# Kernel tuning notes

Hardware: AMD Instinct MI355X
Metric: run time of the kernel (lower is better)

The kernel has to match this reference:

```python
import jax, jax.numpy as jnp
import numpy as np


def setup_inputs() -> dict:
    key = jax.random.key(0)
    k1, k2, k3 = jax.random.split(key, 3)
    Lq, Lkv, H, D = 2048, 2048, 16, 128
    return {
        "query": jax.random.normal(k1, (Lq, H, D), dtype=jnp.float32),
        "key": jax.random.normal(k2, (Lkv, H, D), dtype=jnp.float32),
        "value": jax.random.normal(k3, (Lkv, H, D), dtype=jnp.float32),
    }


def reference(query, key, value):
    # query: [Lq, H, D], key: [Lkv, H, D], value: [Lkv, H, Dv]
    # Original module performs chunked online-softmax attention; the math is
    # exactly scaled-dot-product softmax attention with scale 1/sqrt(k_features).
    d = query.shape[-1]
    q = query * (1.0 / jnp.sqrt(jnp.asarray(d, dtype=query.dtype)))
    scores = jnp.einsum('qhd,khd->qhk', q, key)          # [Lq, H, Lkv]
    weights = jax.nn.softmax(scores, axis=-1)            # numerically stable online softmax equivalent
    out = jnp.einsum('qhk,khf->qhf', weights, value)     # [Lq, H, Dv]
    return out
```

## Files before the change

kernel.cpp:

```cpp
#include <hip/hip_runtime.h>
#include <hip/hip_bf16.h>

typedef __bf16 bf16x8 __attribute__((ext_vector_type(8)));
typedef __bf16 bf16x4 __attribute__((ext_vector_type(4)));
typedef float  f32x16 __attribute__((ext_vector_type(16)));
typedef float  f32x4  __attribute__((ext_vector_type(4)));

#define HD      2048
#define DH      128
#define KVT     64
#define NCH     16
#define NSPLIT  2
#define NROWS   32768
#define KTILE_E 8192
#define VTILE_E 8704

__device__ __forceinline__ void glds16(const void* g, void* l) {
    typedef const __attribute__((address_space(1))) void g_as_t;
    typedef __attribute__((address_space(3))) void l_as_t;
    __builtin_amdgcn_global_load_lds((g_as_t*)g, (l_as_t*)l, 16, 0, 0);
}

__device__ __forceinline__ int kkey_of(int r) {
    return (r & 7) ^ (((r >> 3) & 3) << 1);
}

__global__ __launch_bounds__(256, 4)
void prep_kv(const float* __restrict__ Kg, const float* __restrict__ Vg,
             __bf16* __restrict__ wsK, __bf16* __restrict__ wsV)
{
    __shared__ float tile[32][33];
    const int bid = blockIdx.x;
    if (bid < 2048) {
        const int kv = bid;
        const int t  = threadIdx.x;
        const int h  = t >> 4, c8 = t & 15;
        const float* src = Kg + (size_t)kv * HD + h * DH + c8 * 8;
        f32x4 a = *(const f32x4*)(src);
        f32x4 b = *(const f32x4*)(src + 4);
        bf16x8 o;
        o[0]=(__bf16)a[0]; o[1]=(__bf16)a[1]; o[2]=(__bf16)a[2]; o[3]=(__bf16)a[3];
        o[4]=(__bf16)b[0]; o[5]=(__bf16)b[1]; o[6]=(__bf16)b[2]; o[7]=(__bf16)b[3];
        const int r = kv & 63;
        __bf16* dst = wsK + ((size_t)(h * 32 + (kv >> 6)) * KTILE_E)
                          + r * 128 + ((c8 ^ kkey_of(r)) << 3);
        *(bf16x8*)dst = o;
    } else {
        const int b = bid - 2048;
        const int dvb = b & 3, kvb = (b >> 2) & 63, h = b >> 8;
        const int t = threadIdx.x;
        {
            const int kvl = t >> 3, dv4 = (t & 7) * 4;
            f32x4 v = *(const f32x4*)(Vg + (size_t)(kvb * 32 + kvl) * HD + h * DH + dvb * 32 + dv4);
            tile[kvl][dv4 + 0] = v[0]; tile[kvl][dv4 + 1] = v[1];
            tile[kvl][dv4 + 2] = v[2]; tile[kvl][dv4 + 3] = v[3];
        }
        __syncthreads();
        {
            const int dvl = t >> 3, kv4 = (t & 7) * 4;
            const int dv   = dvb * 32 + dvl;
            const int T    = kvb >> 1;
            const int kloc = (kvb & 1) * 32 + kv4;
            bf16x4 o;
            o[0] = (__bf16)tile[kv4 + 0][dvl]; o[1] = (__bf16)tile[kv4 + 1][dvl];
            o[2] = (__bf16)tile[kv4 + 2][dvl]; o[3] = (__bf16)tile[kv4 + 3][dvl];
            __bf16* dst = wsV + ((size_t)(h * 32 + T) * VTILE_E) + dv * 68 + kloc;
            *(bf16x4*)dst = o;
        }
    }
}

__global__ __launch_bounds__(256, 2)
void fmha_main(const float* __restrict__ Qg,
               const __bf16* __restrict__ wsK, const __bf16* __restrict__ wsV,
               float* __restrict__ wsO, float* __restrict__ wsML)
{
    __shared__ __align__(16) __bf16 klds[2][KTILE_E];
    __shared__ __align__(16) __bf16 vlds[2][VTILE_E];

    const int tid  = threadIdx.x;
    const int lane = tid & 63;
    const int wrp  = tid >> 6;
    const int g    = lane >> 5;
    const int l31  = lane & 31;

    const int b    = blockIdx.x;
    const int grp  = b & 31;
    const int qblk = b >> 5;
    const int h    = grp >> 1;
    const int sp   = grp & 1;
    const int T0   = sp * NCH;

    const float qscale = 1.4426950408889634f * 0.08838834764831845f;
    const int q = qblk * 128 + wrp * 32 + l31;

    bf16x8 qf[8];
    {
        const float* qrow = Qg + (size_t)q * HD + h * DH;
        #pragma unroll
        for (int j = 0; j < 8; ++j) {
            f32x4 a = *(const f32x4*)(qrow + j * 16 + 8 * g);
            f32x4 c = *(const f32x4*)(qrow + j * 16 + 8 * g + 4);
            bf16x8 f;
            f[0] = (__bf16)(a[0] * qscale); f[1] = (__bf16)(a[1] * qscale);
            f[2] = (__bf16)(a[2] * qscale); f[3] = (__bf16)(a[3] * qscale);
            f[4] = (__bf16)(c[0] * qscale); f[5] = (__bf16)(c[1] * qscale);
            f[6] = (__bf16)(c[2] * qscale); f[7] = (__bf16)(c[3] * qscale);
            qf[j] = f;
        }
    }

    auto stage = [&](int T, int buf) {
        const char* kt = (const char*)(wsK + (size_t)(h * 32 + T) * KTILE_E) + wrp * 1024 + lane * 16;
        char* kl = (char*)&klds[buf][0] + wrp * 1024;
        #pragma unroll
        for (int i = 0; i < 4; ++i) glds16(kt + i * 4096, kl + i * 4096);
        const char* vt = (const char*)(wsV + (size_t)(h * 32 + T) * VTILE_E) + wrp * 1024 + lane * 16;
        char* vl = (char*)&vlds[buf][0] + wrp * 1024;
        #pragma unroll
        for (int i = 0; i < 4; ++i) glds16(vt + i * 4096, vl + i * 4096);
        if (wrp == 0) glds16(vt + 16384, vl + 16384);
    };

    auto sync_all = []() {
        asm volatile("s_waitcnt vmcnt(0) lgkmcnt(0)" ::: "memory");
        __builtin_amdgcn_s_barrier();
    };

    float mrun = -1e30f, lrun = 0.0f;
    f32x16 o0, o1, o2, o3;
    #pragma unroll
    for (int r = 0; r < 16; ++r) { o0[r] = 0.f; o1[r] = 0.f; o2[r] = 0.f; o3[r] = 0.f; }

    stage(T0, 0);
    sync_all();

    const int kkey = kkey_of(l31);

    #pragma unroll 2
    for (int tt = 0; tt < NCH; ++tt) {
        const int cur = tt & 1;
        if (tt + 1 < NCH) stage(T0 + tt + 1, cur ^ 1);

        f32x16 s0, s1;
        #pragma unroll
        for (int r = 0; r < 16; ++r) { s0[r] = 0.f; s1[r] = 0.f; }
        __builtin_amdgcn_s_setprio(1);
        #pragma unroll
        for (int j = 0; j < 8; ++j) {
            const int gcol = ((2 * j + g) ^ kkey) << 3;
            bf16x8 k0 = *(const bf16x8*)&klds[cur][l31 * 128 + gcol];
            s0 = __builtin_amdgcn_mfma_f32_32x32x16_bf16(k0, qf[j], s0, 0, 0, 0);
            bf16x8 k1 = *(const bf16x8*)&klds[cur][(32 + l31) * 128 + gcol];
            s1 = __builtin_amdgcn_mfma_f32_32x32x16_bf16(k1, qf[j], s1, 0, 0, 0);
        }
        __builtin_amdgcn_s_setprio(0);

        float m16[8];
        #pragma unroll
        for (int r = 0; r < 8; ++r)
            m16[r] = fmaxf(fmaxf(s0[r], s0[r + 8]), fmaxf(s1[r], s1[r + 8]));
        float tmax = fmaxf(fmaxf(fmaxf(m16[0], m16[4]), fmaxf(m16[1], m16[5])),
                           fmaxf(fmaxf(m16[2], m16[6]), fmaxf(m16[3], m16[7])));
        tmax = fmaxf(tmax, __shfl_xor(tmax, 32, 64));

        if (__any(tmax > mrun + 8.0f)) {
            const float mnew  = fmaxf(mrun, tmax);
            const float alpha = __builtin_amdgcn_exp2f(mrun - mnew);
            lrun *= alpha;
            #pragma unroll
            for (int r = 0; r < 16; ++r) { o0[r]*=alpha; o1[r]*=alpha; o2[r]*=alpha; o3[r]*=alpha; }
            mrun = mnew;
        }

        #pragma unroll
        for (int r = 0; r < 16; ++r) {
            s0[r] = __builtin_amdgcn_exp2f(s0[r] - mrun);
            s1[r] = __builtin_amdgcn_exp2f(s1[r] - mrun);
        }
        float ps = 0.f;
        #pragma unroll
        for (int r = 0; r < 16; ++r) ps += s0[r] + s1[r];
        lrun += ps;

        bf16x8 pf0, pf1, pf2, pf3;
        #pragma unroll
        for (int e = 0; e < 8; ++e) {
            pf0[e] = (__bf16)s0[e]; pf1[e] = (__bf16)s0[8 + e];
            pf2[e] = (__bf16)s1[e]; pf3[e] = (__bf16)s1[8 + e];
        }

        __builtin_amdgcn_s_setprio(1);
        #pragma unroll
        for (int bb = 0; bb < 4; ++bb) {
            const __bf16* vb = &vlds[cur][(bb * 32 + l31) * 68];
            f32x16& oo = (bb == 0) ? o0 : (bb == 1) ? o1 : (bb == 2) ? o2 : o3;
            #define PVSTEP(base, pf)                                              \
            {                                                                     \
                bf16x4 a0 = *(const bf16x4*)(vb + (base) + 4 * g);                \
                bf16x4 a1 = *(const bf16x4*)(vb + (base) + 8 + 4 * g);            \
                bf16x8 va;                                                        \
                va[0]=a0[0]; va[1]=a0[1]; va[2]=a0[2]; va[3]=a0[3];               \
                va[4]=a1[0]; va[5]=a1[1]; va[6]=a1[2]; va[7]=a1[3];               \
                oo = __builtin_amdgcn_mfma_f32_32x32x16_bf16(va, pf, oo, 0, 0, 0);\
            }
            PVSTEP(0,  pf0) PVSTEP(16, pf1) PVSTEP(32, pf2) PVSTEP(48, pf3)
            #undef PVSTEP
        }
        __builtin_amdgcn_s_setprio(0);

        if (tt + 1 < NCH) sync_all();
    }

    const float ltot  = lrun + __shfl_xor(lrun, 32, 64);
    const int   rowid = q * 16 + h;

    float* orow = wsO + ((size_t)sp * NROWS + rowid) * 128;
    #pragma unroll
    for (int bb = 0; bb < 4; ++bb) {
        const f32x16& oo = (bb == 0) ? o0 : (bb == 1) ? o1 : (bb == 2) ? o2 : o3;
        #pragma unroll
        for (int jj = 0; jj < 4; ++jj) {
            f32x4 v;
            v[0] = oo[4*jj+0]; v[1] = oo[4*jj+1]; v[2] = oo[4*jj+2]; v[3] = oo[4*jj+3];
            *(f32x4*)(orow + bb * 32 + 8 * jj + 4 * g) = v;
        }
    }
    if (lane < 32) {
        float* ml = wsML + ((size_t)sp * NROWS + rowid) * 2;
        ml[0] = mrun;
        ml[1] = ltot;
    }
}

__global__ __launch_bounds__(256, 4)
void fmha_combine(const float* __restrict__ wsO, const float* __restrict__ wsML,
                  float* __restrict__ Og)
{
    const int tid   = threadIdx.x;
    const int rowid = blockIdx.x * 8 + (tid >> 5);
    const int c     = (tid & 31) * 4;

    float m[NSPLIT], l[NSPLIT];
    float M = -1e30f;
    #pragma unroll
    for (int s = 0; s < NSPLIT; ++s) {
        const float* ml = wsML + ((size_t)s * NROWS + rowid) * 2;
        m[s] = ml[0]; l[s] = ml[1];
        M = fmaxf(M, m[s]);
    }
    float L = 0.f, w[NSPLIT];
    #pragma unroll
    for (int s = 0; s < NSPLIT; ++s) {
        w[s] = __builtin_amdgcn_exp2f(m[s] - M);
        L += l[s] * w[s];
    }
    const float inv = 1.0f / L;

    f32x4 acc; acc[0]=0.f; acc[1]=0.f; acc[2]=0.f; acc[3]=0.f;
    #pragma unroll
    for (int s = 0; s < NSPLIT; ++s) {
        f32x4 v = *(const f32x4*)(wsO + ((size_t)s * NROWS + rowid) * 128 + c);
        acc[0] += v[0] * w[s]; acc[1] += v[1] * w[s];
        acc[2] += v[2] * w[s]; acc[3] += v[3] * w[s];
    }
    f32x4 r;
    r[0] = acc[0]*inv; r[1] = acc[1]*inv; r[2] = acc[2]*inv; r[3] = acc[3]*inv;
    *(f32x4*)(Og + (size_t)rowid * 128 + c) = r;
}

__global__ __launch_bounds__(256, 2)
void fmha_fb(const float* __restrict__ Qg, const float* __restrict__ Kg,
             const float* __restrict__ Vg, float* __restrict__ Og)
{
    __shared__ __align__(16) __bf16 klds[2][32 * 128];
    __shared__ __align__(16) __bf16 vtlds[2][DH * 36];

    const int tid  = threadIdx.x;
    const int lane = tid & 63;
    const int wrp  = tid >> 6;
    const int g    = lane >> 5;
    const int l31  = lane & 31;

    const int b    = blockIdx.x;
    const int h    = 2 * (b & 7) + ((b >> 3) >> 4);
    const int qblk = (b >> 3) & 15;

    const float qscale = 1.4426950408889634f * 0.08838834764831845f;
    const int q = qblk * 128 + wrp * 32 + l31;

    bf16x8 qf[8];
    {
        const float* qrow = Qg + (size_t)q * HD + h * DH;
        #pragma unroll
        for (int db = 0; db < 8; ++db) {
            f32x4 a = *(const f32x4*)(qrow + db * 16 + 8 * g);
            f32x4 c = *(const f32x4*)(qrow + db * 16 + 8 * g + 4);
            bf16x8 f;
            f[0] = (__bf16)(a[0] * qscale); f[1] = (__bf16)(a[1] * qscale);
            f[2] = (__bf16)(a[2] * qscale); f[3] = (__bf16)(a[3] * qscale);
            f[4] = (__bf16)(c[0] * qscale); f[5] = (__bf16)(c[1] * qscale);
            f[6] = (__bf16)(c[2] * qscale); f[7] = (__bf16)(c[3] * qscale);
            qf[db] = f;
        }
    }

    const int krow = tid >> 3, kc = tid & 7;
    const int vkv  = tid & 31, vdv0 = (tid >> 5) * 16;
    const float* kbase = Kg + (size_t)h * DH;
    const float* vbase = Vg + (size_t)h * DH;

    f32x4 kreg0, kreg1, kreg2, kreg3, vreg0, vreg1, vreg2, vreg3;

    auto stage_load = [&](int t) {
        const float* kp = kbase + (size_t)(t * 32 + krow) * HD + kc * 8;
        kreg0 = *(const f32x4*)(kp);
        kreg1 = *(const f32x4*)(kp + 4);
        kreg2 = *(const f32x4*)(kp + 64);
        kreg3 = *(const f32x4*)(kp + 68);
        const float* vp = vbase + (size_t)(t * 32 + vkv) * HD + vdv0;
        vreg0 = *(const f32x4*)(vp);
        vreg1 = *(const f32x4*)(vp + 4);
        vreg2 = *(const f32x4*)(vp + 8);
        vreg3 = *(const f32x4*)(vp + 12);
    };

    auto stage_write = [&](int buf) {
        bf16x8 k0, k1;
        k0[0]=(__bf16)kreg0[0]; k0[1]=(__bf16)kreg0[1]; k0[2]=(__bf16)kreg0[2]; k0[3]=(__bf16)kreg0[3];
        k0[4]=(__bf16)kreg1[0]; k0[5]=(__bf16)kreg1[1]; k0[6]=(__bf16)kreg1[2]; k0[7]=(__bf16)kreg1[3];
        k1[0]=(__bf16)kreg2[0]; k1[1]=(__bf16)kreg2[1]; k1[2]=(__bf16)kreg2[2]; k1[3]=(__bf16)kreg2[3];
        k1[4]=(__bf16)kreg3[0]; k1[5]=(__bf16)kreg3[1]; k1[6]=(__bf16)kreg3[2]; k1[7]=(__bf16)kreg3[3];
        const int swz = (krow & 7) << 3;
        *(bf16x8*)&klds[buf][krow * 128 + ((kc * 8) ^ swz)]      = k0;
        *(bf16x8*)&klds[buf][krow * 128 + ((kc * 8 + 64) ^ swz)] = k1;
        #pragma unroll
        for (int jj = 0; jj < 4; ++jj) {
            f32x4 vv = (jj == 0) ? vreg0 : (jj == 1) ? vreg1 : (jj == 2) ? vreg2 : vreg3;
            #pragma unroll
            for (int e = 0; e < 4; ++e)
                vtlds[buf][(vdv0 + jj * 4 + e) * 36 + vkv] = (__bf16)vv[e];
        }
    };

    float mrun = -1e30f, lrun = 0.0f;
    f32x16 o0, o1, o2, o3;
    #pragma unroll
    for (int r = 0; r < 16; ++r) { o0[r] = 0.f; o1[r] = 0.f; o2[r] = 0.f; o3[r] = 0.f; }

    stage_load(0);
    stage_write(0);

    for (int tt = 0; tt < 64; ++tt) {
        const int cur = tt & 1;
        if (tt + 1 < 64) stage_load(tt + 1);
        __syncthreads();

        f32x16 sa, sb;
        #pragma unroll
        for (int r = 0; r < 16; ++r) { sa[r] = 0.f; sb[r] = 0.f; }
        const int kswz = (l31 & 7) << 3;
        #pragma unroll
        for (int db = 0; db < 4; ++db) {
            bf16x8 kfa = *(const bf16x8*)&klds[cur][l31 * 128 + (((2*db)   * 16 + g * 8) ^ kswz)];
            sa = __builtin_amdgcn_mfma_f32_32x32x16_bf16(kfa, qf[2*db],   sa, 0, 0, 0);
            bf16x8 kfb = *(const bf16x8*)&klds[cur][l31 * 128 + (((2*db+1) * 16 + g * 8) ^ kswz)];
            sb = __builtin_amdgcn_mfma_f32_32x32x16_bf16(kfb, qf[2*db+1], sb, 0, 0, 0);
        }
        f32x16 s;
        #pragma unroll
        for (int r = 0; r < 16; ++r) s[r] = sa[r] + sb[r];

        float m8[8];
        #pragma unroll
        for (int r = 0; r < 8; ++r) m8[r] = fmaxf(s[r], s[r + 8]);
        float tmax = fmaxf(fmaxf(fmaxf(m8[0], m8[4]), fmaxf(m8[1], m8[5])),
                           fmaxf(fmaxf(m8[2], m8[6]), fmaxf(m8[3], m8[7])));
        tmax = fmaxf(tmax, __shfl_xor(tmax, 32, 64));

        if (__any(tmax > mrun + 8.0f)) {
            const float mnew  = fmaxf(mrun, tmax);
            const float alpha = __builtin_amdgcn_exp2f(mrun - mnew);
            lrun *= alpha;
            #pragma unroll
            for (int r = 0; r < 16; ++r) { o0[r] *= alpha; o1[r] *= alpha; o2[r] *= alpha; o3[r] *= alpha; }
            mrun = mnew;
        }

        float p[16];
        #pragma unroll
        for (int r = 0; r < 16; ++r) p[r] = __builtin_amdgcn_exp2f(s[r] - mrun);
        float ps0 = 0, ps1 = 0, ps2 = 0, ps3 = 0;
        #pragma unroll
        for (int r = 0; r < 4; ++r) { ps0 += p[r]; ps1 += p[r+4]; ps2 += p[r+8]; ps3 += p[r+12]; }
        lrun += ((ps0 + ps1) + (ps2 + ps3));

        bf16x8 pf0, pf1;
        #pragma unroll
        for (int e = 0; e < 8; ++e) { pf0[e] = (__bf16)p[e]; pf1[e] = (__bf16)p[8 + e]; }

        #pragma unroll
        for (int bb = 0; bb < 4; ++bb) {
            const __bf16* vb = &vtlds[cur][(bb * 32 + l31) * 36];
            bf16x4 a0 = *(const bf16x4*)(vb + 4 * g);
            bf16x4 a1 = *(const bf16x4*)(vb + 8 + 4 * g);
            bf16x8 va;
            va[0]=a0[0]; va[1]=a0[1]; va[2]=a0[2]; va[3]=a0[3];
            va[4]=a1[0]; va[5]=a1[1]; va[6]=a1[2]; va[7]=a1[3];
            f32x16& oo = (bb == 0) ? o0 : (bb == 1) ? o1 : (bb == 2) ? o2 : o3;
            oo = __builtin_amdgcn_mfma_f32_32x32x16_bf16(va, pf0, oo, 0, 0, 0);
            bf16x4 b0 = *(const bf16x4*)(vb + 16 + 4 * g);
            bf16x4 b1 = *(const bf16x4*)(vb + 24 + 4 * g);
            va[0]=b0[0]; va[1]=b0[1]; va[2]=b0[2]; va[3]=b0[3];
            va[4]=b1[0]; va[5]=b1[1]; va[6]=b1[2]; va[7]=b1[3];
            oo = __builtin_amdgcn_mfma_f32_32x32x16_bf16(va, pf1, oo, 0, 0, 0);
        }

        if (tt + 1 < 64) stage_write(cur ^ 1);
    }

    const float ltot = lrun + __shfl_xor(lrun, 32, 64);
    const float inv  = 1.0f / ltot;
    float* orow = Og + ((size_t)q * 16 + h) * 128;
    #pragma unroll
    for (int bb = 0; bb < 4; ++bb) {
        const f32x16& oo = (bb == 0) ? o0 : (bb == 1) ? o1 : (bb == 2) ? o2 : o3;
        #pragma unroll
        for (int jj = 0; jj < 4; ++jj) {
            f32x4 v;
            v[0] = oo[4*jj+0] * inv; v[1] = oo[4*jj+1] * inv;
            v[2] = oo[4*jj+2] * inv; v[3] = oo[4*jj+3] * inv;
            *(f32x4*)(orow + bb * 32 + 8 * jj + 4 * g) = v;
        }
    }
}

extern "C" void kernel_launch(void* const* d_in, const int* in_sizes, int n_in,
                              void* d_out, int out_size, void* d_ws, size_t ws_size,
                              hipStream_t stream) {
    const float* Q = (const float*)d_in[0];
    const float* K = (const float*)d_in[1];
    const float* V = (const float*)d_in[2];
    float* O = (float*)d_out;

    const size_t wsK_b = (size_t)512 * KTILE_E * 2;
    const size_t wsV_b = (size_t)512 * VTILE_E * 2;
    const size_t needO  = (size_t)NSPLIT * NROWS * 128;
    const size_t needML = (size_t)NSPLIT * NROWS * 2;
    const size_t need_bytes = wsK_b + wsV_b + (needO + needML) * sizeof(float);

    if (ws_size >= need_bytes) {
        __bf16* wsK = (__bf16*)d_ws;
        __bf16* wsV = (__bf16*)((char*)d_ws + wsK_b);
        float*  wsO = (float*)((char*)d_ws + wsK_b + wsV_b);
        float*  wsML = wsO + needO;
        hipLaunchKernelGGL(prep_kv, dim3(6144), dim3(256), 0, stream, K, V, wsK, wsV);
        hipLaunchKernelGGL(fmha_main, dim3(512), dim3(256), 0, stream,
                           Q, wsK, wsV, wsO, wsML);
        hipLaunchKernelGGL(fmha_combine, dim3(NROWS / 8), dim3(256), 0, stream,
                           wsO, wsML, O);
    } else {
        hipLaunchKernelGGL(fmha_fb, dim3(256), dim3(256), 0, stream, Q, K, V, O);
    }
}
```

Before: 71.99 us.

## Use 32-row KV tiles, three-way KV split, and bf16 partial outputs

Halves the KV tile to 32 rows, splitting the QK^T reduction into two accumulators over halves of the head dimension. The KV range is split three ways (22/21/21 tiles), launching 768 blocks instead of 512 to fill the CUs better, with launch bounds raised to 3 blocks per CU. Partial outputs are written as bf16 instead of fp32 to cut workspace traffic in the combine kernel, at some accuracy cost. More loop iterations and barriers per block add synchronisation overhead.

```diff
diff --git a/kernel.cpp b/kernel.cpp
--- a/kernel.cpp
+++ b/kernel.cpp
@@ -8,12 +8,13 @@
 
 #define HD      2048
 #define DH      128
-#define KVT     64
-#define NCH     16
-#define NSPLIT  2
+#define KVT     32
+#define NSPLIT  3
 #define NROWS   32768
-#define KTILE_E 8192
-#define VTILE_E 8704
+#define KTILE_E 4096
+#define KTILE_B 8192
+#define VTILE_E 4608
+#define VTILE_B 9216
 
 __device__ __forceinline__ void glds16(const void* g, void* l) {
     typedef const __attribute__((address_space(1))) void g_as_t;
@@ -41,8 +42,8 @@
         bf16x8 o;
         o[0]=(__bf16)a[0]; o[1]=(__bf16)a[1]; o[2]=(__bf16)a[2]; o[3]=(__bf16)a[3];
         o[4]=(__bf16)b[0]; o[5]=(__bf16)b[1]; o[6]=(__bf16)b[2]; o[7]=(__bf16)b[3];
-        const int r = kv & 63;
-        __bf16* dst = wsK + ((size_t)(h * 32 + (kv >> 6)) * KTILE_E)
+        const int r = kv & 31;
+        __bf16* dst = wsK + ((size_t)(h * 64 + (kv >> 5)) * KTILE_E)
                           + r * 128 + ((c8 ^ kkey_of(r)) << 3);
         *(bf16x8*)dst = o;
     } else {
@@ -58,22 +59,20 @@
         __syncthreads();
         {
             const int dvl = t >> 3, kv4 = (t & 7) * 4;
-            const int dv   = dvb * 32 + dvl;
-            const int T    = kvb >> 1;
-            const int kloc = (kvb & 1) * 32 + kv4;
+            const int dv = dvb * 32 + dvl;
             bf16x4 o;
             o[0] = (__bf16)tile[kv4 + 0][dvl]; o[1] = (__bf16)tile[kv4 + 1][dvl];
             o[2] = (__bf16)tile[kv4 + 2][dvl]; o[3] = (__bf16)tile[kv4 + 3][dvl];
-            __bf16* dst = wsV + ((size_t)(h * 32 + T) * VTILE_E) + dv * 68 + kloc;
+            __bf16* dst = wsV + ((size_t)(h * 64 + kvb) * VTILE_E) + dv * 36 + kv4;
             *(bf16x4*)dst = o;
         }
     }
 }
 
-__global__ __launch_bounds__(256, 2)
+__global__ __launch_bounds__(256, 3)
 void fmha_main(const float* __restrict__ Qg,
                const __bf16* __restrict__ wsK, const __bf16* __restrict__ wsV,
-               float* __restrict__ wsO, float* __restrict__ wsML)
+               __bf16* __restrict__ wsOb, float* __restrict__ wsML)
 {
     __shared__ __align__(16) __bf16 klds[2][KTILE_E];
     __shared__ __align__(16) __bf16 vlds[2][VTILE_E];
@@ -85,14 +84,15 @@
     const int l31  = lane & 31;
 
     const int b    = blockIdx.x;
-    const int grp  = b & 31;
-    const int qblk = b >> 5;
-    const int h    = grp >> 1;
-    const int sp   = grp & 1;
-    const int T0   = sp * NCH;
+    const int grp  = b % 48;
+    const int qb   = b / 48;
+    const int h    = grp / 3;
+    const int sp   = grp % 3;
+    const int t0   = (sp == 0) ? 0 : (22 + 21 * (sp - 1));
+    const int nch  = (sp == 0) ? 22 : 21;
 
     const float qscale = 1.4426950408889634f * 0.08838834764831845f;
-    const int q = qblk * 128 + wrp * 32 + l31;
+    const int q = qb * 128 + wrp * 32 + l31;
 
     bf16x8 qf[8];
     {
@@ -111,15 +111,15 @@
     }
 
     auto stage = [&](int T, int buf) {
-        const char* kt = (const char*)(wsK + (size_t)(h * 32 + T) * KTILE_E) + wrp * 1024 + lane * 16;
+        const char* kt = (const char*)wsK + (size_t)(h * 64 + T) * KTILE_B + wrp * 1024 + lane * 16;
         char* kl = (char*)&klds[buf][0] + wrp * 1024;
-        #pragma unroll
-        for (int i = 0; i < 4; ++i) glds16(kt + i * 4096, kl + i * 4096);
-        const char* vt = (const char*)(wsV + (size_t)(h * 32 + T) * VTILE_E) + wrp * 1024 + lane * 16;
+        glds16(kt, kl);
+        glds16(kt + 4096, kl + 4096);
+        const char* vt = (const char*)wsV + (size_t)(h * 64 + T) * VTILE_B + wrp * 1024 + lane * 16;
         char* vl = (char*)&vlds[buf][0] + wrp * 1024;
-        #pragma unroll
-        for (int i = 0; i < 4; ++i) glds16(vt + i * 4096, vl + i * 4096);
-        if (wrp == 0) glds16(vt + 16384, vl + 16384);
+        glds16(vt, vl);
+        glds16(vt + 4096, vl + 4096);
+        if (wrp == 0) glds16(vt + 8192, vl + 8192);
     };
 
     auto sync_all = []() {
@@ -132,36 +132,37 @@
     #pragma unroll
     for (int r = 0; r < 16; ++r) { o0[r] = 0.f; o1[r] = 0.f; o2[r] = 0.f; o3[r] = 0.f; }
 
-    stage(T0, 0);
+    stage(t0, 0);
     sync_all();
 
     const int kkey = kkey_of(l31);
 
     #pragma unroll 2
-    for (int tt = 0; tt < NCH; ++tt) {
+    for (int tt = 0; tt < nch; ++tt) {
         const int cur = tt & 1;
-        if (tt + 1 < NCH) stage(T0 + tt + 1, cur ^ 1);
-
-        f32x16 s0, s1;
-        #pragma unroll
-        for (int r = 0; r < 16; ++r) { s0[r] = 0.f; s1[r] = 0.f; }
+        if (tt + 1 < nch) stage(t0 + tt + 1, cur ^ 1);
+
+        f32x16 sa, sb;
+        #pragma unroll
+        for (int r = 0; r < 16; ++r) { sa[r] = 0.f; sb[r] = 0.f; }
         __builtin_amdgcn_s_setprio(1);
         #pragma unroll
-        for (int j = 0; j < 8; ++j) {
-            const int gcol = ((2 * j + g) ^ kkey) << 3;
-            bf16x8 k0 = *(const bf16x8*)&klds[cur][l31 * 128 + gcol];
-            s0 = __builtin_amdgcn_mfma_f32_32x32x16_bf16(k0, qf[j], s0, 0, 0, 0);
-            bf16x8 k1 = *(const bf16x8*)&klds[cur][(32 + l31) * 128 + gcol];
-            s1 = __builtin_amdgcn_mfma_f32_32x32x16_bf16(k1, qf[j], s1, 0, 0, 0);
+        for (int j = 0; j < 4; ++j) {
+            bf16x8 ka = *(const bf16x8*)&klds[cur][l31 * 128 + (((2*j       + g) ^ kkey) << 3)];
+            sa = __builtin_amdgcn_mfma_f32_32x32x16_bf16(ka, qf[j],     sa, 0, 0, 0);
+            bf16x8 kb = *(const bf16x8*)&klds[cur][l31 * 128 + (((2*(j+4) + g) ^ kkey) << 3)];
+            sb = __builtin_amdgcn_mfma_f32_32x32x16_bf16(kb, qf[j + 4], sb, 0, 0, 0);
         }
         __builtin_amdgcn_s_setprio(0);
-
-        float m16[8];
-        #pragma unroll
-        for (int r = 0; r < 8; ++r)
-            m16[r] = fmaxf(fmaxf(s0[r], s0[r + 8]), fmaxf(s1[r], s1[r + 8]));
-        float tmax = fmaxf(fmaxf(fmaxf(m16[0], m16[4]), fmaxf(m16[1], m16[5])),
-                           fmaxf(fmaxf(m16[2], m16[6]), fmaxf(m16[3], m16[7])));
+        f32x16 s;
+        #pragma unroll
+        for (int r = 0; r < 16; ++r) s[r] = sa[r] + sb[r];
+
+        float m8[8];
+        #pragma unroll
+        for (int r = 0; r < 8; ++r) m8[r] = fmaxf(s[r], s[r + 8]);
+        float tmax = fmaxf(fmaxf(fmaxf(m8[0], m8[4]), fmaxf(m8[1], m8[5])),
+                           fmaxf(fmaxf(m8[2], m8[6]), fmaxf(m8[3], m8[7])));
         tmax = fmaxf(tmax, __shfl_xor(tmax, 32, 64));
 
         if (__any(tmax > mrun + 8.0f)) {
@@ -174,56 +175,51 @@
         }
 
         #pragma unroll
-        for (int r = 0; r < 16; ++r) {
-            s0[r] = __builtin_amdgcn_exp2f(s0[r] - mrun);
-            s1[r] = __builtin_amdgcn_exp2f(s1[r] - mrun);
-        }
+        for (int r = 0; r < 16; ++r) s[r] = __builtin_amdgcn_exp2f(s[r] - mrun);
         float ps = 0.f;
         #pragma unroll
-        for (int r = 0; r < 16; ++r) ps += s0[r] + s1[r];
+        for (int r = 0; r < 16; ++r) ps += s[r];
         lrun += ps;
 
-        bf16x8 pf0, pf1, pf2, pf3;
-        #pragma unroll
-        for (int e = 0; e < 8; ++e) {
-            pf0[e] = (__bf16)s0[e]; pf1[e] = (__bf16)s0[8 + e];
-            pf2[e] = (__bf16)s1[e]; pf3[e] = (__bf16)s1[8 + e];
-        }
+        bf16x8 pf0, pf1;
+        #pragma unroll
+        for (int e = 0; e < 8; ++e) { pf0[e] = (__bf16)s[e]; pf1[e] = (__bf16)s[8 + e]; }
 
         __builtin_amdgcn_s_setprio(1);
         #pragma unroll
         for (int bb = 0; bb < 4; ++bb) {
-            const __bf16* vb = &vlds[cur][(bb * 32 + l31) * 68];
+            const __bf16* vb = &vlds[cur][(bb * 32 + l31) * 36];
             f32x16& oo = (bb == 0) ? o0 : (bb == 1) ? o1 : (bb == 2) ? o2 : o3;
-            #define PVSTEP(base, pf)                                              \
-            {                                                                     \
-                bf16x4 a0 = *(const bf16x4*)(vb + (base) + 4 * g);                \
-                bf16x4 a1 = *(const bf16x4*)(vb + (base) + 8 + 4 * g);            \
-                bf16x8 va;                                                        \
-                va[0]=a0[0]; va[1]=a0[1]; va[2]=a0[2]; va[3]=a0[3];               \
-                va[4]=a1[0]; va[5]=a1[1]; va[6]=a1[2]; va[7]=a1[3];               \
-                oo = __builtin_amdgcn_mfma_f32_32x32x16_bf16(va, pf, oo, 0, 0, 0);\
-            }
-            PVSTEP(0,  pf0) PVSTEP(16, pf1) PVSTEP(32, pf2) PVSTEP(48, pf3)
-            #undef PVSTEP
+            bf16x4 a0 = *(const bf16x4*)(vb + 4 * g);
+            bf16x4 a1 = *(const bf16x4*)(vb + 8 + 4 * g);
+            bf16x8 va;
+            va[0]=a0[0]; va[1]=a0[1]; va[2]=a0[2]; va[3]=a0[3];
+            va[4]=a1[0]; va[5]=a1[1]; va[6]=a1[2]; va[7]=a1[3];
+            oo = __builtin_amdgcn_mfma_f32_32x32x16_bf16(va, pf0, oo, 0, 0, 0);
+            bf16x4 b0 = *(const bf16x4*)(vb + 16 + 4 * g);
+            bf16x4 b1 = *(const bf16x4*)(vb + 24 + 4 * g);
+            va[0]=b0[0]; va[1]=b0[1]; va[2]=b0[2]; va[3]=b0[3];
+            va[4]=b1[0]; va[5]=b1[1]; va[6]=b1[2]; va[7]=b1[3];
+            oo = __builtin_amdgcn_mfma_f32_32x32x16_bf16(va, pf1, oo, 0, 0, 0);
         }
         __builtin_amdgcn_s_setprio(0);
 
-        if (tt + 1 < NCH) sync_all();
+        if (tt + 1 < nch) sync_all();
     }
 
     const float ltot  = lrun + __shfl_xor(lrun, 32, 64);
     const int   rowid = q * 16 + h;
 
-    float* orow = wsO + ((size_t)sp * NROWS + rowid) * 128;
+    __bf16* orow = wsOb + ((size_t)sp * NROWS + rowid) * 128;
     #pragma unroll
     for (int bb = 0; bb < 4; ++bb) {
         const f32x16& oo = (bb == 0) ? o0 : (bb == 1) ? o1 : (bb == 2) ? o2 : o3;
         #pragma unroll
         for (int jj = 0; jj < 4; ++jj) {
-            f32x4 v;
-            v[0] = oo[4*jj+0]; v[1] = oo[4*jj+1]; v[2] = oo[4*jj+2]; v[3] = oo[4*jj+3];
-            *(f32x4*)(orow + bb * 32 + 8 * jj + 4 * g) = v;
+            bf16x4 v;
+            v[0] = (__bf16)oo[4*jj+0]; v[1] = (__bf16)oo[4*jj+1];
+            v[2] = (__bf16)oo[4*jj+2]; v[3] = (__bf16)oo[4*jj+3];
+            *(bf16x4*)(orow + bb * 32 + 8 * jj + 4 * g) = v;
         }
     }
     if (lane < 32) {
@@ -234,7 +230,7 @@
 }
 
 __global__ __launch_bounds__(256, 4)
-void fmha_combine(const float* __restrict__ wsO, const float* __restrict__ wsML,
+void fmha_combine(const __bf16* __restrict__ wsOb, const float* __restrict__ wsML,
                   float* __restrict__ Og)
 {
     const int tid   = threadIdx.x;
@@ -260,9 +256,9 @@
     f32x4 acc; acc[0]=0.f; acc[1]=0.f; acc[2]=0.f; acc[3]=0.f;
     #pragma unroll
     for (int s = 0; s < NSPLIT; ++s) {
-        f32x4 v = *(const f32x4*)(wsO + ((size_t)s * NROWS + rowid) * 128 + c);
-        acc[0] += v[0] * w[s]; acc[1] += v[1] * w[s];
-        acc[2] += v[2] * w[s]; acc[3] += v[3] * w[s];
+        bf16x4 v = *(const bf16x4*)(wsOb + ((size_t)s * NROWS + rowid) * 128 + c);
+        acc[0] += (float)v[0] * w[s]; acc[1] += (float)v[1] * w[s];
+        acc[2] += (float)v[2] * w[s]; acc[3] += (float)v[3] * w[s];
     }
     f32x4 r;
     r[0] = acc[0]*inv; r[1] = acc[1]*inv; r[2] = acc[2]*inv; r[3] = acc[3]*inv;
@@ -443,22 +439,22 @@
     const float* V = (const float*)d_in[2];
     float* O = (float*)d_out;
 
-    const size_t wsK_b = (size_t)512 * KTILE_E * 2;
-    const size_t wsV_b = (size_t)512 * VTILE_E * 2;
-    const size_t needO  = (size_t)NSPLIT * NROWS * 128;
-    const size_t needML = (size_t)NSPLIT * NROWS * 2;
-    const size_t need_bytes = wsK_b + wsV_b + (needO + needML) * sizeof(float);
+    const size_t wsK_b  = (size_t)16 * 64 * KTILE_B;
+    const size_t wsV_b  = (size_t)16 * 64 * VTILE_B;
+    const size_t wsOb_b = (size_t)NSPLIT * NROWS * 128 * 2;
+    const size_t wsML_b = (size_t)NSPLIT * NROWS * 2 * 4;
+    const size_t need_bytes = wsK_b + wsV_b + wsOb_b + wsML_b;
 
     if (ws_size >= need_bytes) {
-        __bf16* wsK = (__bf16*)d_ws;
-        __bf16* wsV = (__bf16*)((char*)d_ws + wsK_b);
-        float*  wsO = (float*)((char*)d_ws + wsK_b + wsV_b);
-        float*  wsML = wsO + needO;
+        __bf16* wsK  = (__bf16*)d_ws;
+        __bf16* wsV  = (__bf16*)((char*)d_ws + wsK_b);
+        __bf16* wsOb = (__bf16*)((char*)d_ws + wsK_b + wsV_b);
+        float*  wsML = (float*)((char*)d_ws + wsK_b + wsV_b + wsOb_b);
         hipLaunchKernelGGL(prep_kv, dim3(6144), dim3(256), 0, stream, K, V, wsK, wsV);
-        hipLaunchKernelGGL(fmha_main, dim3(512), dim3(256), 0, stream,
-                           Q, wsK, wsV, wsO, wsML);
+        hipLaunchKernelGGL(fmha_main, dim3(768), dim3(256), 0, stream,
+                           Q, wsK, wsV, wsOb, wsML);
         hipLaunchKernelGGL(fmha_combine, dim3(NROWS / 8), dim3(256), 0, stream,
-                           wsO, wsML, O);
+                           wsOb, wsML, O);
     } else {
         hipLaunchKernelGGL(fmha_fb, dim3(256), dim3(256), 0, stream, Q, K, V, O);
     }
```

Measured after the change: 75.37 us. 4.7% more time.
